# Kernel tuning notes

Hardware: AMD Instinct MI355X
Metric: run time of the kernel (lower is better)

Reference implementation:

```python
import jax, jax.numpy as jnp
import numpy as np

N_HEAD = 16  # head_dim = C // N_HEAD = 128


def setup_inputs() -> dict:
    key = jax.random.key(0)
    k1, k2, k3 = jax.random.split(key, 3)
    B, T, C = 2, 2048, 2048
    x = jax.random.normal(k1, (B, T, C), dtype=jnp.float32)
    # c_attn: Linear(C, 3*C), no bias; stored as (in, out) for x @ W
    w_attn = jax.random.normal(k2, (C, 3 * C), dtype=jnp.float32) * (1.0 / np.sqrt(C))
    # c_proj: Linear(C, C), no bias
    w_proj = jax.random.normal(k3, (C, C), dtype=jnp.float32) * (1.0 / np.sqrt(C))
    return {"x": x, "w_attn": w_attn, "w_proj": w_proj}


def reference(x, w_attn, w_proj):
    B, T, C = x.shape
    H = N_HEAD
    D = C // H  # head dimension
    qkv = x @ w_attn                      # [B, T, 3C]
    q, k, v = jnp.split(qkv, 3, axis=-1)  # each [B, T, C]
    # [B, T, C] -> [B, H, T, D]
    q = q.reshape(B, T, H, D).transpose(0, 2, 1, 3)
    k = k.reshape(B, T, H, D).transpose(0, 2, 1, 3)
    v = v.reshape(B, T, H, D).transpose(0, 2, 1, 3)
    scale = 1.0 / np.sqrt(D).astype(np.float32)
    att = jnp.einsum('bhqd,bhkd->bhqk', q, k) * scale  # [B, H, T, T]
    causal = jnp.tril(jnp.ones((T, T), dtype=bool))
    att = jnp.where(causal[None, None, :, :], att, jnp.float32(-jnp.inf))
    att = jax.nn.softmax(att, axis=-1)
    y = jnp.einsum('bhqk,bhkd->bhqd', att, v)  # [B, H, T, D]
    y = y.transpose(0, 2, 1, 3).reshape(B, T, C)
    # all_reduce is identity with number_of_workers=1; dropout=0 (eval)
    return y @ w_proj
```

## Files before the change

### kernel.cpp

```cpp
#include <hip/hip_runtime.h>
#include <hip/hip_bf16.h>
#include <stdint.h>

#define TLEN 2048
#define CDIM 2048
#define BDIM 2
#define HDIM 16
#define DHEAD 128
#define QROW ((size_t)(3 * CDIM))

typedef __bf16 bf16x8 __attribute__((ext_vector_type(8)));
typedef float f32x4 __attribute__((ext_vector_type(4)));

__device__ __forceinline__ uint16_t f32_to_bf16(float f) {
    uint32_t u = __builtin_bit_cast(uint32_t, f);
    uint32_t r = (u + 0x7FFFu + ((u >> 16) & 1u)) >> 16;
    return (uint16_t)r;
}
__device__ __forceinline__ float bf16_to_f32(uint32_t h) {
    uint32_t u = h << 16;
    return __builtin_bit_cast(float, u);
}

__device__ __forceinline__ void gload_lds16(const uint16_t* g, uint16_t* l) {
    __builtin_amdgcn_global_load_lds(
        (const __attribute__((address_space(1))) uint32_t*)g,
        (__attribute__((address_space(3))) uint32_t*)l, 16, 0, 0);
}

__global__ void cvt_f32_bf16(const float* __restrict__ in, uint16_t* __restrict__ out, int n) {
    int i = (blockIdx.x * blockDim.x + threadIdx.x) * 4;
    if (i + 3 < n) {
        float4 f = *reinterpret_cast<const float4*>(in + i);
        ushort4 o;
        o.x = f32_to_bf16(f.x);
        o.y = f32_to_bf16(f.y);
        o.z = f32_to_bf16(f.z);
        o.w = f32_to_bf16(f.w);
        *reinterpret_cast<ushort4*>(out + i) = o;
    }
}

__global__ __launch_bounds__(256) void transpose_cvt(const float* __restrict__ in,
                                                     uint16_t* __restrict__ out,
                                                     int R, int Cc) {
    __shared__ uint16_t tile[64][65];
    int c0 = blockIdx.x * 64;
    int r0 = blockIdx.y * 64;
    int tc = threadIdx.x & 63;
    int t4 = threadIdx.x >> 6;
    for (int rr = t4; rr < 64; rr += 4) {
        tile[rr][tc] = f32_to_bf16(in[(size_t)(r0 + rr) * Cc + c0 + tc]);
    }
    __syncthreads();
    int wr = threadIdx.x & 63;
    for (int cc = t4; cc < 64; cc += 4) {
        out[(size_t)(c0 + cc) * R + r0 + wr] = tile[wr][cc];
    }
}

template <int MODE>
__global__ __launch_bounds__(256) void gemm_bf16_128(const uint16_t* __restrict__ A,
                                                     const uint16_t* __restrict__ Bt,
                                                     void* __restrict__ Cp,
                                                     uint16_t* __restrict__ vt,
                                                     int M, int N, int K) {
    __shared__ __align__(16) uint16_t As[128 * 32];
    __shared__ __align__(16) uint16_t Bs[128 * 32];
    const int tid = threadIdx.x;
    const int wave = tid >> 6;
    const int lane = tid & 63;
    const int l15 = lane & 15;
    const int quad = lane >> 4;
    const int m0 = blockIdx.y * 128;
    const int n0 = blockIdx.x * 128;
    const int wm = (wave >> 1) * 64;
    const int wn = (wave & 1) * 64;

    f32x4 acc[4][4] = {};

    const int s0 = wave * 2;
    const int lrow = lane >> 2;
    const int swzW = (lrow ^ (lrow >> 2)) & 3;
    const int cblk = (lane & 3) ^ swzW;
    const uint16_t* Ag = A + (size_t)(m0 + s0 * 16 + lrow) * K + cblk * 8;
    const uint16_t* Bg = Bt + (size_t)(n0 + s0 * 16 + lrow) * K + cblk * 8;
    uint16_t* AsW0 = As + s0 * 512;
    uint16_t* AsW1 = As + (s0 + 1) * 512;
    uint16_t* BsW0 = Bs + s0 * 512;
    uint16_t* BsW1 = Bs + (s0 + 1) * 512;
    const size_t rowStep = (size_t)16 * K;

    const int swzR = (l15 ^ (l15 >> 2)) & 3;
    const int rdblk = (quad ^ swzR) * 8;

    for (int k0 = 0; k0 < K; k0 += 32) {
        gload_lds16(Ag + k0, AsW0);
        gload_lds16(Ag + rowStep + k0, AsW1);
        gload_lds16(Bg + k0, BsW0);
        gload_lds16(Bg + rowStep + k0, BsW1);
        __syncthreads();

        bf16x8 af[4], bfr[4];
#pragma unroll
        for (int mi = 0; mi < 4; mi++)
            af[mi] = *reinterpret_cast<const bf16x8*>(
                As + (wm + mi * 16 + l15) * 32 + rdblk);
#pragma unroll
        for (int ni = 0; ni < 4; ni++)
            bfr[ni] = *reinterpret_cast<const bf16x8*>(
                Bs + (wn + ni * 16 + l15) * 32 + rdblk);
#pragma unroll
        for (int mi = 0; mi < 4; mi++)
#pragma unroll
            for (int ni = 0; ni < 4; ni++)
                acc[mi][ni] = __builtin_amdgcn_mfma_f32_16x16x32_bf16(
                    af[mi], bfr[ni], acc[mi][ni], 0, 0, 0);
        __syncthreads();
    }

    const bool vmode = (MODE == 2) && (n0 >= 2 * CDIM);
#pragma unroll
    for (int mi = 0; mi < 4; mi++)
#pragma unroll
        for (int ni = 0; ni < 4; ni++) {
            if (vmode) {
                int col = n0 + wn + ni * 16 + l15;
                int vcol = col - 2 * CDIM;
                int hh = vcol >> 7, d = vcol & 127;
                int rowm = m0 + wm + mi * 16 + quad * 4;
                int bb = rowm >> 11, t = rowm & 2047;
                uint32_t lo = (uint32_t)f32_to_bf16(acc[mi][ni][0]) |
                              ((uint32_t)f32_to_bf16(acc[mi][ni][1]) << 16);
                uint32_t hi = (uint32_t)f32_to_bf16(acc[mi][ni][2]) |
                              ((uint32_t)f32_to_bf16(acc[mi][ni][3]) << 16);
                *reinterpret_cast<uint2*>(
                    vt + ((size_t)((bb * HDIM + hh) * DHEAD + d)) * TLEN + t) =
                    make_uint2(lo, hi);
            } else {
#pragma unroll
                for (int r = 0; r < 4; r++) {
                    int row = m0 + wm + mi * 16 + quad * 4 + r;
                    int col = n0 + wn + ni * 16 + l15;
                    float v = acc[mi][ni][r];
                    if (MODE != 0)
                        ((uint16_t*)Cp)[(size_t)row * N + col] = f32_to_bf16(v);
                    else
                        ((float*)Cp)[(size_t)row * N + col] = v;
                }
            }
        }
}

#define ATT_C1 0.12751743f
#define ATT_C2 17.3123405f

__global__ __launch_bounds__(256) void attn_mfma3(const uint16_t* __restrict__ qkv,
                                                  const uint16_t* __restrict__ vtg,
                                                  uint16_t* __restrict__ y) {
    __shared__ __align__(16) uint16_t Ks[64 * 128];
    __shared__ __align__(16) uint16_t Vts[128 * 64];
    __shared__ __align__(16) uint16_t Ps[4][32 * 72];

    const int tid = threadIdx.x;
    const int wave = tid >> 6;
    const int lane = tid & 63;
    const int l15 = lane & 15;
    const int quad = lane >> 4;
    const int h = blockIdx.y;
    const int b = blockIdx.z;
    const int qblk = (int)gridDim.x - 1 - (int)blockIdx.x;
    const int qbase = qblk * 128 + wave * 32;
    const int kmax = qbase + 31;

    const uint16_t* kg = qkv + (size_t)b * TLEN * QROW + CDIM + h * DHEAD;
    const uint16_t* vg = vtg + (size_t)(b * HDIM + h) * DHEAD * TLEN;
    uint16_t* PsW = Ps[wave];

    int koff[4], voff[4];
#pragma unroll
    for (int i = 0; i < 4; i++) {
        int Lb = (wave * 4 + i) * 64 + lane;
        int key = Lb >> 4;
        int ck = (Lb & 15) ^ (key & 15);
        koff[i] = key * (int)QROW + ck * 8;
        int d = Lb >> 3;
        int cv = (Lb & 7) ^ (d & 7);
        voff[i] = d * TLEN + cv * 8;
    }

    bf16x8 qfrag[2][4];
#pragma unroll
    for (int m = 0; m < 2; m++) {
        const uint16_t* qp =
            qkv + (size_t)(b * TLEN + qbase + m * 16 + l15) * QROW + h * DHEAD + quad * 8;
#pragma unroll
        for (int kc = 0; kc < 4; kc++)
            qfrag[m][kc] = *reinterpret_cast<const bf16x8*>(qp + kc * 32);
    }

    f32x4 oacc[2][8] = {};
    float psum[2] = {0.f, 0.f};

    const int diagT = qblk * 2 + (wave >> 1);
    const int ntiles = qblk * 2 + 2;

    for (int t = 0; t < ntiles; t++) {
        const int j0 = t * 64;
        if (t > 0) __syncthreads();
        {
            const uint16_t* kj = kg + (size_t)j0 * QROW;
            const uint16_t* vj = vg + j0;
#pragma unroll
            for (int i = 0; i < 4; i++) {
                gload_lds16(kj + koff[i], Ks + (wave * 4 + i) * 512);
                gload_lds16(vj + voff[i], Vts + (wave * 4 + i) * 512);
            }
        }
        __syncthreads();
        if (t > diagT) continue;

        const bool masked = (t == diagT);
        const int n0max = masked ? ((kmax - j0) >> 4) : 3;

        f32x4 st[4][2];
#pragma unroll
        for (int n0 = 0; n0 < 4; n0++) {
            if (masked && n0 > n0max) continue;
            bf16x8 kf[4];
#pragma unroll
            for (int kc = 0; kc < 4; kc++) {
                int cpr = (kc * 4 + quad) ^ l15;
                kf[kc] = *reinterpret_cast<const bf16x8*>(
                    Ks + (n0 * 16 + l15) * 128 + cpr * 8);
            }
#pragma unroll
            for (int m = 0; m < 2; m++) {
                f32x4 acc = {};
#pragma unroll
                for (int kc = 0; kc < 4; kc++)
                    acc = __builtin_amdgcn_mfma_f32_16x16x32_bf16(
                        kf[kc], qfrag[m][kc], acc, 0, 0, 0);
                st[n0][m] = acc;
            }
        }

#pragma unroll
        for (int n0 = 0; n0 < 4; n0++) {
            if (masked && n0 > n0max) continue;
#pragma unroll
            for (int m = 0; m < 2; m++) {
                uint32_t pk0, pk1;
                float pv[4];
#pragma unroll
                for (int r = 0; r < 4; r++) {
                    float p = exp2f(st[n0][m][r] * ATT_C1 - ATT_C2);
                    if (masked) {
                        int key = j0 + n0 * 16 + quad * 4 + r;
                        int q = qbase + m * 16 + l15;
                        if (key > q) p = 0.f;
                    }
                    uint32_t pb = f32_to_bf16(p);
                    pv[r] = bf16_to_f32(pb);
                    if (r == 0) pk0 = pb;
                    else if (r == 1) pk0 |= pb << 16;
                    else if (r == 2) pk1 = pb;
                    else pk1 |= pb << 16;
                }
                psum[m] += (pv[0] + pv[1]) + (pv[2] + pv[3]);
                *reinterpret_cast<uint2*>(PsW + (m * 16 + l15) * 72 + n0 * 16 + quad * 4) =
                    make_uint2(pk0, pk1);
            }
        }

        const int kcend = masked ? (((kmax - j0) >> 5) + 1) : 2;
#pragma unroll
        for (int kc = 0; kc < 2; kc++) {
            if (kc >= kcend) continue;
            bf16x8 pf[2];
#pragma unroll
            for (int m = 0; m < 2; m++)
                pf[m] = *reinterpret_cast<const bf16x8*>(
                    PsW + (m * 16 + l15) * 72 + kc * 32 + quad * 8);
#pragma unroll
            for (int n0 = 0; n0 < 8; n0++) {
                int cpr = (kc * 4 + quad) ^ (l15 & 7);
                bf16x8 vf = *reinterpret_cast<const bf16x8*>(
                    Vts + (n0 * 16 + l15) * 64 + cpr * 8);
#pragma unroll
                for (int m = 0; m < 2; m++)
                    oacc[m][n0] = __builtin_amdgcn_mfma_f32_16x16x32_bf16(
                        pf[m], vf, oacc[m][n0], 0, 0, 0);
            }
        }
    }

#pragma unroll
    for (int m = 0; m < 2; m++) {
        float s = psum[m];
        s += __shfl_xor(s, 16);
        s += __shfl_xor(s, 32);
        psum[m] = 1.0f / s;
    }
    uint16_t* ybase = y + (size_t)(b * TLEN + qbase) * CDIM + h * DHEAD;
#pragma unroll
    for (int m = 0; m < 2; m++)
#pragma unroll
        for (int r = 0; r < 4; r++) {
            float inv = __shfl(psum[m], quad * 4 + r);
#pragma unroll
            for (int n0 = 0; n0 < 8; n0++)
                ybase[(size_t)(m * 16 + quad * 4 + r) * CDIM + n0 * 16 + l15] =
                    f32_to_bf16(oacc[m][n0][r] * inv);
        }
}

extern "C" void kernel_launch(void* const* d_in, const int* in_sizes, int n_in,
                              void* d_out, int out_size, void* d_ws, size_t ws_size,
                              hipStream_t stream) {
    const float* x = (const float*)d_in[0];
    const float* w_attn = (const float*)d_in[1];
    const float* w_proj = (const float*)d_in[2];
    float* out = (float*)d_out;

    const int M = BDIM * TLEN;
    const int K = CDIM;
    const int N3 = 3 * CDIM;

    char* ws = (char*)d_ws;
    uint16_t* xb = (uint16_t*)(ws);
    uint16_t* waT = (uint16_t*)(ws + 16777216);
    uint16_t* wpT = (uint16_t*)(ws + 41943040);
    uint16_t* qkvb = (uint16_t*)(ws + 50331648);
    uint16_t* yb = (uint16_t*)(ws + 100663296);
    uint16_t* vtb = xb;

    cvt_f32_bf16<<<(M * K / 4 + 255) / 256, 256, 0, stream>>>(x, xb, M * K);
    transpose_cvt<<<dim3(N3 / 64, K / 64), 256, 0, stream>>>(w_attn, waT, K, N3);
    transpose_cvt<<<dim3(K / 64, K / 64), 256, 0, stream>>>(w_proj, wpT, K, K);
    gemm_bf16_128<2><<<dim3(N3 / 128, M / 128), 256, 0, stream>>>(xb, waT, (void*)qkvb, vtb, M, N3, K);
    attn_mfma3<<<dim3(TLEN / 128, HDIM, BDIM), 256, 0, stream>>>(qkvb, vtb, yb);
    gemm_bf16_128<0><<<dim3(K / 128, M / 128), 256, 0, stream>>>(yb, wpT, (void*)out, nullptr, M, K, K);
}
```

Before: 446.4 us.

## Add 256x256 double-buffered GEMM with direct-to-LDS loads for QKV projection

Introduces a new 512-thread GEMM kernel with 256x256 output tiles, double-buffered LDS filled by global_load_lds with XOR swizzling, phased MFMA/load interleaving with barriers and priority hints, and an XCD-aware block remap. The QKV projection uses it, and the Q/K output is stored compactly with a 2C row stride while V goes to a separate transposed buffer instead of aliasing xb. This targets the global-memory latency and LDS stalls of the smaller 128x128 single-buffered GEMM. In exchange it uses 128KB of LDS and a large register footprint, which limits occupancy, and the manual waitcnt scheduling is fragile.

```diff
diff --git a/kernel.cpp b/kernel.cpp
--- a/kernel.cpp
+++ b/kernel.cpp
@@ -7,7 +7,7 @@
 #define BDIM 2
 #define HDIM 16
 #define DHEAD 128
-#define QROW ((size_t)(3 * CDIM))
+#define QROW ((size_t)(2 * CDIM))
 
 typedef __bf16 bf16x8 __attribute__((ext_vector_type(8)));
 typedef float f32x4 __attribute__((ext_vector_type(4)));
@@ -57,6 +57,164 @@
     for (int cc = t4; cc < 64; cc += 4) {
         out[(size_t)(c0 + cc) * R + r0 + wr] = tile[wr][cc];
     }
+}
+
+
+#define RD8(P, OFF) (*reinterpret_cast<const bf16x8*>((P) + (OFF)))
+
+#define PH_RDA(CA, MB)                                        \
+    _Pragma("unroll") for (int mi = 0; mi < 4; mi++) {        \
+        af[mi][0] = RD8(CA, rdA + ((MB) + mi) * 1024 + kblk0); \
+        af[mi][1] = RD8(CA, rdA + ((MB) + mi) * 1024 + kblk1); \
+    }
+
+#define PH_RDB(CB, NIB)                                              \
+    _Pragma("unroll") for (int ni = 0; ni < 2; ni++) {               \
+        bf[(NIB) + ni][0] = RD8(CB, rdB + ((NIB) + ni) * 1024 + kblk0); \
+        bf[(NIB) + ni][1] = RD8(CB, rdB + ((NIB) + ni) * 1024 + kblk1); \
+    }
+
+#define PH_MFMA(MB, NIB)                                                        \
+    __builtin_amdgcn_s_barrier();                                               \
+    asm volatile("s_waitcnt lgkmcnt(0)" ::: "memory");                          \
+    __builtin_amdgcn_s_setprio(1);                                              \
+    _Pragma("unroll") for (int mi = 0; mi < 4; mi++)                            \
+    _Pragma("unroll") for (int ni = 0; ni < 2; ni++) {                          \
+        acc[(MB) + mi][(NIB) + ni] = __builtin_amdgcn_mfma_f32_16x16x32_bf16(   \
+            af[mi][0], bf[(NIB) + ni][0], acc[(MB) + mi][(NIB) + ni], 0, 0, 0); \
+        acc[(MB) + mi][(NIB) + ni] = __builtin_amdgcn_mfma_f32_16x16x32_bf16(   \
+            af[mi][1], bf[(NIB) + ni][1], acc[(MB) + mi][(NIB) + ni], 0, 0, 0); \
+    }                                                                           \
+    __builtin_amdgcn_s_setprio(0);                                              \
+    __builtin_amdgcn_s_barrier();                                               \
+    __builtin_amdgcn_sched_barrier(0);
+
+#define TILE(T, CA, CB, NA, NB)                              \
+    {                                                        \
+        const int k0 = (T) * 64;                             \
+        PH_RDA(CA, 0)                                        \
+        PH_RDB(CB, 0)                                        \
+        if ((T) + 1 < nt) stB(NB, 1, k0 + 64);               \
+        PH_MFMA(0, 0)                                        \
+        PH_RDB(CB, 2)                                        \
+        if ((T) + 1 < nt) stA(NA, 1, k0 + 64);               \
+        PH_MFMA(0, 2)                                        \
+        PH_RDA(CA, 4)                                        \
+        if ((T) + 2 < nt) stB(CB, 0, k0 + 128);              \
+        PH_MFMA(4, 2)                                        \
+        if ((T) + 2 < nt) {                                  \
+            stA(CA, 0, k0 + 128);                            \
+            asm volatile("s_waitcnt vmcnt(4)" ::: "memory"); \
+        } else if ((T) + 1 < nt) {                           \
+            asm volatile("s_waitcnt vmcnt(0)" ::: "memory"); \
+        }                                                    \
+        PH_MFMA(4, 0)                                        \
+    }
+
+template <int MODE>
+__global__ __launch_bounds__(512, 2) void gemm_bf16_256(const uint16_t* __restrict__ A,
+                                                        const uint16_t* __restrict__ Bt,
+                                                        void* __restrict__ Cp,
+                                                        uint16_t* __restrict__ vt,
+                                                        int M, int N, int K) {
+    __shared__ __align__(16) uint16_t lds[65536];
+    uint16_t* const As0 = lds;
+    uint16_t* const Bs0 = lds + 16384;
+    uint16_t* const As1 = lds + 32768;
+    uint16_t* const Bs1 = lds + 49152;
+
+    const int tid = threadIdx.x;
+    const int wave = tid >> 6;
+    const int lane = tid & 63;
+    const int l15 = lane & 15;
+    const int quad = lane >> 4;
+    const int wrow = wave >> 2;
+    const int wcol = wave & 3;
+
+    const int gx = gridDim.x;
+    const int nwg = gx * gridDim.y;
+    const int flat = blockIdx.y * gx + blockIdx.x;
+    const int cpx = nwg >> 3;
+    const int id2 = (flat & 7) * cpx + (flat >> 3);
+    const int n0 = (id2 % gx) * 256;
+    const int m0 = (id2 / gx) * 256;
+
+    const int srow = wave * 8 + (lane >> 3);
+    const int scol = ((lane & 7) ^ (lane >> 3)) * 8;
+    const uint16_t* Ag = A + (size_t)(m0 + srow) * K + scol;
+    const uint16_t* Bg = Bt + (size_t)(n0 + srow) * K + scol;
+    const int ldsoff = wave * 512;
+
+    const int rdA = (wrow * 128 + l15) * 64;
+    const int rdB = (wcol * 64 + l15) * 64;
+    const int kblk0 = (quad ^ (l15 & 7)) * 8;
+    const int kblk1 = ((4 + quad) ^ (l15 & 7)) * 8;
+
+    const int nt = K >> 6;
+    f32x4 acc[8][4] = {};
+    bf16x8 af[4][2], bf[4][2];
+
+    auto stA = [&](uint16_t* dstb, int hf, int kk) {
+        const uint16_t* s = Ag + (size_t)(hf * 128) * K + kk;
+        uint16_t* d = dstb + hf * 8192 + ldsoff;
+        gload_lds16(s, d);
+        gload_lds16(s + (size_t)64 * K, d + 4096);
+    };
+    auto stB = [&](uint16_t* dstb, int hf, int kk) {
+        const uint16_t* s = Bg + (size_t)(hf * 128) * K + kk;
+        uint16_t* d = dstb + hf * 8192 + ldsoff;
+        gload_lds16(s, d);
+        gload_lds16(s + (size_t)64 * K, d + 4096);
+    };
+
+    stB(Bs0, 0, 0);
+    stA(As0, 0, 0);
+    stB(Bs0, 1, 0);
+    stA(As0, 1, 0);
+    stB(Bs1, 0, 64);
+    stA(As1, 0, 64);
+    asm volatile("s_waitcnt vmcnt(4)" ::: "memory");
+    __builtin_amdgcn_s_barrier();
+    __builtin_amdgcn_sched_barrier(0);
+
+    for (int t = 0; t < nt; t += 2) {
+        TILE(t, As0, Bs0, As1, Bs1)
+        TILE(t + 1, As1, Bs1, As0, Bs0)
+    }
+
+    const bool vmode = (MODE == 2) && (n0 >= 2 * CDIM);
+#pragma unroll
+    for (int mi = 0; mi < 8; mi++)
+#pragma unroll
+        for (int ni = 0; ni < 4; ni++) {
+            if (vmode) {
+                int col = n0 + wcol * 64 + ni * 16 + l15;
+                int vcol = col - 2 * CDIM;
+                int hh = vcol >> 7, d = vcol & 127;
+                int rowm = m0 + wrow * 128 + mi * 16 + quad * 4;
+                int bb = rowm >> 11, tt = rowm & 2047;
+                uint32_t lo = (uint32_t)f32_to_bf16(acc[mi][ni][0]) |
+                              ((uint32_t)f32_to_bf16(acc[mi][ni][1]) << 16);
+                uint32_t hi = (uint32_t)f32_to_bf16(acc[mi][ni][2]) |
+                              ((uint32_t)f32_to_bf16(acc[mi][ni][3]) << 16);
+                *reinterpret_cast<uint2*>(
+                    vt + ((size_t)((bb * HDIM + hh) * DHEAD + d)) * TLEN + tt) =
+                    make_uint2(lo, hi);
+            } else {
+#pragma unroll
+                for (int r = 0; r < 4; r++) {
+                    int row = m0 + wrow * 128 + mi * 16 + quad * 4 + r;
+                    int col = n0 + wcol * 64 + ni * 16 + l15;
+                    float v = acc[mi][ni][r];
+                    if (MODE == 2)
+                        ((uint16_t*)Cp)[(size_t)row * (2 * CDIM) + col] = f32_to_bf16(v);
+                    else if (MODE == 1)
+                        ((uint16_t*)Cp)[(size_t)row * N + col] = f32_to_bf16(v);
+                    else
+                        ((float*)Cp)[(size_t)row * N + col] = v;
+                }
+            }
+        }
 }
 
 template <int MODE>
@@ -119,35 +277,19 @@
         __syncthreads();
     }
 
-    const bool vmode = (MODE == 2) && (n0 >= 2 * CDIM);
 #pragma unroll
     for (int mi = 0; mi < 4; mi++)
 #pragma unroll
         for (int ni = 0; ni < 4; ni++) {
-            if (vmode) {
+#pragma unroll
+            for (int r = 0; r < 4; r++) {
+                int row = m0 + wm + mi * 16 + quad * 4 + r;
                 int col = n0 + wn + ni * 16 + l15;
-                int vcol = col - 2 * CDIM;
-                int hh = vcol >> 7, d = vcol & 127;
-                int rowm = m0 + wm + mi * 16 + quad * 4;
-                int bb = rowm >> 11, t = rowm & 2047;
-                uint32_t lo = (uint32_t)f32_to_bf16(acc[mi][ni][0]) |
-                              ((uint32_t)f32_to_bf16(acc[mi][ni][1]) << 16);
-                uint32_t hi = (uint32_t)f32_to_bf16(acc[mi][ni][2]) |
-                              ((uint32_t)f32_to_bf16(acc[mi][ni][3]) << 16);
-                *reinterpret_cast<uint2*>(
-                    vt + ((size_t)((bb * HDIM + hh) * DHEAD + d)) * TLEN + t) =
-                    make_uint2(lo, hi);
-            } else {
-#pragma unroll
-                for (int r = 0; r < 4; r++) {
-                    int row = m0 + wm + mi * 16 + quad * 4 + r;
-                    int col = n0 + wn + ni * 16 + l15;
-                    float v = acc[mi][ni][r];
-                    if (MODE != 0)
-                        ((uint16_t*)Cp)[(size_t)row * N + col] = f32_to_bf16(v);
-                    else
-                        ((float*)Cp)[(size_t)row * N + col] = v;
-                }
+                float v = acc[mi][ni][r];
+                if (MODE != 0)
+                    ((uint16_t*)Cp)[(size_t)row * N + col] = f32_to_bf16(v);
+                else
+                    ((float*)Cp)[(size_t)row * N + col] = v;
             }
         }
 }
@@ -331,14 +473,14 @@
     uint16_t* xb = (uint16_t*)(ws);
     uint16_t* waT = (uint16_t*)(ws + 16777216);
     uint16_t* wpT = (uint16_t*)(ws + 41943040);
-    uint16_t* qkvb = (uint16_t*)(ws + 50331648);
+    uint16_t* qkp = (uint16_t*)(ws + 50331648);
+    uint16_t* vtb = (uint16_t*)(ws + 83886080);
     uint16_t* yb = (uint16_t*)(ws + 100663296);
-    uint16_t* vtb = xb;
 
     cvt_f32_bf16<<<(M * K / 4 + 255) / 256, 256, 0, stream>>>(x, xb, M * K);
     transpose_cvt<<<dim3(N3 / 64, K / 64), 256, 0, stream>>>(w_attn, waT, K, N3);
     transpose_cvt<<<dim3(K / 64, K / 64), 256, 0, stream>>>(w_proj, wpT, K, K);
-    gemm_bf16_128<2><<<dim3(N3 / 128, M / 128), 256, 0, stream>>>(xb, waT, (void*)qkvb, vtb, M, N3, K);
-    attn_mfma3<<<dim3(TLEN / 128, HDIM, BDIM), 256, 0, stream>>>(qkvb, vtb, yb);
+    gemm_bf16_256<2><<<dim3(N3 / 256, M / 256), 512, 0, stream>>>(xb, waT, (void*)qkp, vtb, M, N3, K);
+    attn_mfma3<<<dim3(TLEN / 128, HDIM, BDIM), 256, 0, stream>>>(qkp, vtb, yb);
     gemm_bf16_128<0><<<dim3(K / 128, M / 128), 256, 0, stream>>>(yb, wpT, (void*)out, nullptr, M, K, K);
 }
```

Result: no change. 438.0 us (-1.9%).
